# Performance work log

Hardware: AMD Instinct MI355X
Metric: run time of the kernel (lower is better)

## Reference

```python
import jax, jax.numpy as jnp
import numpy as np

GT_MASK_LEN = 128   # processor_dct.gt_mask_len
N_KEEP = 256        # processor_dct.n_keep


def _zigzag_flat_positions(n):
    """Row-major flat index of the k-th element in JPEG zigzag order of an n x n grid."""
    order = []
    for s in range(2 * n - 1):
        if s % 2 == 0:  # even diagonals traverse up-right
            for i in range(min(s, n - 1), max(-1, s - n), -1):
                order.append((i, s - i))
        else:
            for j in range(min(s, n - 1), max(-1, s - n), -1):
                order.append((s - j, j))
    return np.array([i * n + j for (i, j) in order], dtype=np.int64)


def _dct_matrix(n):
    """Orthonormal DCT-II matrix C (cv2.dct). cv2.idct(Y) == C.T @ Y @ C in 2-D."""
    k = np.arange(n)[:, None].astype(np.float64)
    m = np.arange(n)[None, :].astype(np.float64)
    C = np.sqrt(2.0 / n) * np.cos(np.pi * (2 * m + 1) * k / (2 * n))
    C[0, :] = np.sqrt(1.0 / n)
    return C.astype(np.float32)

_ZZ_POS = jnp.asarray(_zigzag_flat_positions(GT_MASK_LEN)[:N_KEEP])
_DCT_C = jnp.asarray(_dct_matrix(GT_MASK_LEN))


def setup_inputs() -> dict:
    key = jax.random.key(0)
    k1, k2, k3, k4 = jax.random.split(key, 4)
    B, R, C = 8, 300, 91
    pred_logits = jax.random.normal(k1, (B, R, C), dtype=jnp.float32)
    pred_boxes = jax.random.uniform(k2, (B, R, 4), dtype=jnp.float32) * 0.5 + 0.25
    pred_vectors = jax.random.normal(k3, (B, R, N_KEEP), dtype=jnp.float32)
    target_sizes = jax.random.randint(k4, (B, 2), 512, 1334, dtype=jnp.int32)
    return {"pred_logits": pred_logits, "pred_boxes": pred_boxes,
            "pred_vectors": pred_vectors, "target_sizes": target_sizes}


def reference(pred_logits, pred_boxes, pred_vectors, target_sizes):
    L = GT_MASK_LEN
    # --- classification scores ---
    prob = jax.nn.sigmoid(pred_logits)            # [B,R,C]
    scores = prob.max(axis=2)                     # [B,R]
    labels = prob.argmax(axis=2)                  # [B,R] int
    # --- boxes: cxcywh -> xyxy, rescale to image size ---
    cx, cy, w, h = jnp.split(pred_boxes, 4, axis=-1)
    boxes = jnp.concatenate([cx - 0.5 * w, cy - 0.5 * h,
                             cx + 0.5 * w, cy + 0.5 * h], axis=-1)  # [B,R,4]
    ts = target_sizes.astype(jnp.float32)
    img_h, img_w = ts[:, 0], ts[:, 1]
    scale_fct = jnp.stack([img_w, img_h, img_w, img_h], axis=1)     # [B,4]
    boxes = boxes * scale_fct[:, None, :]
    # --- masks: inverse zigzag scatter + batched separable 2-D IDCT ---
    B, R, _ = pred_vectors.shape
    flat = jnp.zeros((B, R, L * L), dtype=pred_vectors.dtype)
    flat = flat.at[:, :, _ZZ_POS].set(pred_vectors)
    coef = flat.reshape(B, R, L, L)
    # cv2.idct(Y) = C^T Y C (orthonormal DCT-III)
    re_mask = jnp.einsum('iu,bruv,vj->brij', _DCT_C.T, coef, _DCT_C)  # [B,R,L,L]
    max_v = re_mask.max(axis=(-2, -1), keepdims=True)
    min_v = re_mask.min(axis=(-2, -1), keepdims=True)
    masks = jnp.where(re_mask > (max_v + min_v) * 0.5, 1.0, 0.0).astype(jnp.float32)
    return scores, labels, boxes, masks
```

## Files before the change

kernel.cpp:

```cpp
#include <hip/hip_runtime.h>
#include <math.h>

#define NROWS 2400
#define NCLS  91
#define L     128
#define KSUB  23
#define NKEEP 256

#define Z_OFF 5888
#define SMEM_FLOATS 6912

__global__ void __launch_bounds__(256)
postproc_kernel(const float* __restrict__ logits,
                const float* __restrict__ pboxes,
                const float* __restrict__ vecs,
                const int*   __restrict__ tsz,
                float* __restrict__ out)
{
    __shared__ float smem[SMEM_FLOATS];
    const int br  = blockIdx.x;
    const int tid = threadIdx.x;

    if (tid < 64) {
        const float* lrow = logits + (size_t)br * NCLS;
        float p = 1.0f / (1.0f + expf(-lrow[tid]));
        int   bi = tid;
        if (tid < NCLS - 64) {
            float p2 = 1.0f / (1.0f + expf(-lrow[tid + 64]));
            if (p2 > p) { p = p2; bi = tid + 64; }
        }
        #pragma unroll
        for (int off = 32; off > 0; off >>= 1) {
            float po = __shfl_xor(p, off, 64);
            int   io = __shfl_xor(bi, off, 64);
            if (po > p || (po == p && io < bi)) { p = po; bi = io; }
        }
        if (tid == 0) {
            out[br] = p;
            out[NROWS + br] = (float)bi;
            const int b = br / 300;
            const float W = (float)tsz[2 * b + 1];
            const float H = (float)tsz[2 * b + 0];
            const float4 bx = *(const float4*)(pboxes + (size_t)br * 4);
            float4 o;
            o.x = (bx.x - 0.5f * bx.z) * W;
            o.y = (bx.y - 0.5f * bx.w) * H;
            o.z = (bx.x + 0.5f * bx.z) * W;
            o.w = (bx.y + 0.5f * bx.w) * H;
            *(float4*)(out + 2 * NROWS + (size_t)br * 4) = o;
        }
    }

    double* tab = (double*)&smem[Z_OFF];
    for (int t = tid; t < 512; t += 256)
        tab[t] = cos((3.14159265358979323846 / 256.0) * (double)t);
    __syncthreads();
    {
        const double s0 = sqrt(1.0 / 128.0);
        for (int idx = tid; idx < KSUB * L; idx += 256) {
            const int u = idx >> 7, m = idx & 127;
            float v;
            if (u == 0) v = (float)s0;
            else        v = (float)(0.125 * tab[((2 * m + 1) * u) & 511]);
            smem[idx] = v;
        }
    }
    __syncthreads();

    float* coef = &smem[Z_OFF];
    for (int idx = tid; idx < KSUB * 24; idx += 256) coef[idx] = 0.0f;
    __syncthreads();
    {
        const int k = tid;
        int s = 0;
        while ((s + 1) * (s + 2) / 2 <= k) ++s;
        const int r = k - s * (s + 1) / 2;
        const int u  = (s & 1) ? r : (s - r);
        const int vv = (s & 1) ? (s - r) : r;
        coef[u * 24 + vv] = vecs[(size_t)br * NKEEP + k];
    }
    __syncthreads();

    float* M1 = &smem[2944];
    for (int t = tid; t < KSUB * 32; t += 256) {
        const int v = t >> 5, i4 = (t & 31) << 2;
        float4 a = make_float4(0.f, 0.f, 0.f, 0.f);
        #pragma unroll
        for (int u = 0; u < KSUB; ++u) {
            const float4 cs = *(const float4*)&smem[u * L + i4];
            const float  cf = coef[u * 24 + v];
            a.x += cs.x * cf; a.y += cs.y * cf; a.z += cs.z * cf; a.w += cs.w * cf;
        }
        *(float4*)&M1[v * L + i4] = a;
    }
    __syncthreads();

    const int tx = tid & 31, ty = tid >> 5;
    const int j0 = tx << 2, i0 = ty << 4;
    float acc[16][4];
    #pragma unroll
    for (int r = 0; r < 16; ++r)
        #pragma unroll
        for (int q = 0; q < 4; ++q) acc[r][q] = 0.0f;

    for (int v = 0; v < KSUB; ++v) {
        const float4 c  = *(const float4*)&smem[v * L + j0];
        const float4 m0 = *(const float4*)&M1[v * L + i0];
        const float4 m1 = *(const float4*)&M1[v * L + i0 + 4];
        const float4 m2 = *(const float4*)&M1[v * L + i0 + 8];
        const float4 m3 = *(const float4*)&M1[v * L + i0 + 12];
        const float mv[16] = { m0.x, m0.y, m0.z, m0.w,
                               m1.x, m1.y, m1.z, m1.w,
                               m2.x, m2.y, m2.z, m2.w,
                               m3.x, m3.y, m3.z, m3.w };
        #pragma unroll
        for (int r = 0; r < 16; ++r) {
            acc[r][0] += mv[r] * c.x;
            acc[r][1] += mv[r] * c.y;
            acc[r][2] += mv[r] * c.z;
            acc[r][3] += mv[r] * c.w;
        }
    }

    float mn = acc[0][0], mx = acc[0][0];
    #pragma unroll
    for (int r = 0; r < 16; ++r)
        #pragma unroll
        for (int q = 0; q < 4; ++q) {
            mn = fminf(mn, acc[r][q]);
            mx = fmaxf(mx, acc[r][q]);
        }
    #pragma unroll
    for (int off = 32; off > 0; off >>= 1) {
        mn = fminf(mn, __shfl_xor(mn, off, 64));
        mx = fmaxf(mx, __shfl_xor(mx, off, 64));
    }
    const int w = tid >> 6;
    if ((tid & 63) == 0) { smem[Z_OFF + w] = mn; smem[Z_OFF + 4 + w] = mx; }
    __syncthreads();
    const float gmn = fminf(fminf(smem[Z_OFF + 0], smem[Z_OFF + 1]),
                            fminf(smem[Z_OFF + 2], smem[Z_OFF + 3]));
    const float gmx = fmaxf(fmaxf(smem[Z_OFF + 4], smem[Z_OFF + 5]),
                            fmaxf(smem[Z_OFF + 6], smem[Z_OFF + 7]));
    const float thr = (gmx + gmn) * 0.5f;

    float* omask = out + 6 * NROWS + (size_t)br * (L * L);
    #pragma unroll
    for (int r = 0; r < 16; ++r) {
        float4 o;
        o.x = acc[r][0] > thr ? 1.0f : 0.0f;
        o.y = acc[r][1] > thr ? 1.0f : 0.0f;
        o.z = acc[r][2] > thr ? 1.0f : 0.0f;
        o.w = acc[r][3] > thr ? 1.0f : 0.0f;
        *(float4*)&omask[(i0 + r) * L + j0] = o;
    }
}

extern "C" void kernel_launch(void* const* d_in, const int* in_sizes, int n_in,
                              void* d_out, int out_size, void* d_ws, size_t ws_size,
                              hipStream_t stream)
{
    const float* logits = (const float*)d_in[0];
    const float* pboxes = (const float*)d_in[1];
    const float* vecs   = (const float*)d_in[2];
    const int*   tsz    = (const int*)d_in[3];
    float* out = (float*)d_out;
    (void)d_ws; (void)ws_size; (void)in_sizes; (void)n_in; (void)out_size;

    postproc_kernel<<<dim3(NROWS), dim3(256), 0, stream>>>(logits, pboxes, vecs, tsz, out);
}
```

Before: 193.3 us.

## Precompute DCT basis in a setup kernel and restructure first IDCT pass

Moves the per-block double-precision cosine table and DCT basis construction into a small one-block kernel that writes the basis to workspace. Each main block then copies the basis from global memory, so it no longer evaluates double cos. The change also removes two barriers by zeroing only the coefficient slots the scatter will not write, and it rewrites the first matmul pass so each thread keeps a basis column in registers. The cost is an extra kernel launch and a dependency between the two kernels.

```diff
diff --git a/kernel.cpp b/kernel.cpp
--- a/kernel.cpp
+++ b/kernel.cpp
@@ -7,14 +7,34 @@
 #define KSUB  23
 #define NKEEP 256
 
-#define Z_OFF 5888
-#define SMEM_FLOATS 6912
+__global__ void __launch_bounds__(256)
+build_csub_kernel(float* __restrict__ csub)
+{
+    __shared__ double tab[512];
+    const int tid = threadIdx.x;
+    for (int t = tid; t < 512; t += 256)
+        tab[t] = cos((3.14159265358979323846 / 256.0) * (double)t);
+    __syncthreads();
+    const double s0 = sqrt(1.0 / 128.0);
+    for (int idx = tid; idx < KSUB * L; idx += 256) {
+        const int u = idx >> 7, m = idx & 127;
+        float v;
+        if (u == 0) v = (float)s0;
+        else        v = (float)(0.125 * tab[((2 * m + 1) * u) & 511]);
+        csub[idx] = v;
+    }
+}
+
+#define COEF_OFF 5888
+#define RED_OFF  6440
+#define SMEM_FLOATS 6448
 
 __global__ void __launch_bounds__(256)
 postproc_kernel(const float* __restrict__ logits,
                 const float* __restrict__ pboxes,
                 const float* __restrict__ vecs,
                 const int*   __restrict__ tsz,
+                const float* __restrict__ csub_g,
                 float* __restrict__ out)
 {
     __shared__ float smem[SMEM_FLOATS];
@@ -51,25 +71,15 @@
         }
     }
 
-    double* tab = (double*)&smem[Z_OFF];
-    for (int t = tid; t < 512; t += 256)
-        tab[t] = cos((3.14159265358979323846 / 256.0) * (double)t);
-    __syncthreads();
-    {
-        const double s0 = sqrt(1.0 / 128.0);
-        for (int idx = tid; idx < KSUB * L; idx += 256) {
-            const int u = idx >> 7, m = idx & 127;
-            float v;
-            if (u == 0) v = (float)s0;
-            else        v = (float)(0.125 * tab[((2 * m + 1) * u) & 511]);
-            smem[idx] = v;
-        }
+    for (int t = tid; t < 736; t += 256)
+        ((float4*)smem)[t] = ((const float4*)csub_g)[t];
+
+    float* coef = &smem[COEF_OFF];
+    for (int t = tid; t < KSUB * 24; t += 256) {
+        const int u = t / 24, v = t - u * 24;
+        const int s = u + v;
+        if (v == 23 || s > 22 || (s == 22 && u < 20)) coef[t] = 0.0f;
     }
-    __syncthreads();
-
-    float* coef = &smem[Z_OFF];
-    for (int idx = tid; idx < KSUB * 24; idx += 256) coef[idx] = 0.0f;
-    __syncthreads();
     {
         const int k = tid;
         int s = 0;
@@ -82,16 +92,28 @@
     __syncthreads();
 
     float* M1 = &smem[2944];
-    for (int t = tid; t < KSUB * 32; t += 256) {
-        const int v = t >> 5, i4 = (t & 31) << 2;
-        float4 a = make_float4(0.f, 0.f, 0.f, 0.f);
+    {
+        const int i = tid & 127;
+        float cs[KSUB];
         #pragma unroll
-        for (int u = 0; u < KSUB; ++u) {
-            const float4 cs = *(const float4*)&smem[u * L + i4];
-            const float  cf = coef[u * 24 + v];
-            a.x += cs.x * cf; a.y += cs.y * cf; a.z += cs.z * cf; a.w += cs.w * cf;
+        for (int u = 0; u < KSUB; ++u) cs[u] = smem[u * L + i];
+        if (tid < 128) {
+            #pragma unroll
+            for (int v = 0; v < 12; ++v) {
+                float a = 0.0f;
+                #pragma unroll
+                for (int u = 0; u < KSUB; ++u) a += cs[u] * coef[u * 24 + v];
+                M1[v * L + i] = a;
+            }
+        } else {
+            #pragma unroll
+            for (int v = 12; v < KSUB; ++v) {
+                float a = 0.0f;
+                #pragma unroll
+                for (int u = 0; u < KSUB; ++u) a += cs[u] * coef[u * 24 + v];
+                M1[v * L + i] = a;
+            }
         }
-        *(float4*)&M1[v * L + i4] = a;
     }
     __syncthreads();
 
@@ -136,12 +158,12 @@
         mx = fmaxf(mx, __shfl_xor(mx, off, 64));
     }
     const int w = tid >> 6;
-    if ((tid & 63) == 0) { smem[Z_OFF + w] = mn; smem[Z_OFF + 4 + w] = mx; }
+    if ((tid & 63) == 0) { smem[RED_OFF + w] = mn; smem[RED_OFF + 4 + w] = mx; }
     __syncthreads();
-    const float gmn = fminf(fminf(smem[Z_OFF + 0], smem[Z_OFF + 1]),
-                            fminf(smem[Z_OFF + 2], smem[Z_OFF + 3]));
-    const float gmx = fmaxf(fmaxf(smem[Z_OFF + 4], smem[Z_OFF + 5]),
-                            fmaxf(smem[Z_OFF + 6], smem[Z_OFF + 7]));
+    const float gmn = fminf(fminf(smem[RED_OFF + 0], smem[RED_OFF + 1]),
+                            fminf(smem[RED_OFF + 2], smem[RED_OFF + 3]));
+    const float gmx = fmaxf(fmaxf(smem[RED_OFF + 4], smem[RED_OFF + 5]),
+                            fmaxf(smem[RED_OFF + 6], smem[RED_OFF + 7]));
     const float thr = (gmx + gmn) * 0.5f;
 
     float* omask = out + 6 * NROWS + (size_t)br * (L * L);
@@ -164,8 +186,10 @@
     const float* pboxes = (const float*)d_in[1];
     const float* vecs   = (const float*)d_in[2];
     const int*   tsz    = (const int*)d_in[3];
-    float* out = (float*)d_out;
-    (void)d_ws; (void)ws_size; (void)in_sizes; (void)n_in; (void)out_size;
+    float* out  = (float*)d_out;
+    float* csub = (float*)d_ws;
+    (void)in_sizes; (void)n_in; (void)out_size; (void)ws_size;
 
-    postproc_kernel<<<dim3(NROWS), dim3(256), 0, stream>>>(logits, pboxes, vecs, tsz, out);
+    build_csub_kernel<<<dim3(1), dim3(256), 0, stream>>>(csub);
+    postproc_kernel<<<dim3(NROWS), dim3(256), 0, stream>>>(logits, pboxes, vecs, tsz, csub, out);
 }
```

New measurement: 197.7 us. 1.02x slower.

## Compute the separable IDCT with bf16 MFMA and 512-thread blocks

Applied to the files above, without the earlier changes.

Replaces the two FP32 scalar matrix-multiply stages of the 2-D IDCT with bf16 16x16x32 MFMA instructions. The DCT basis and scattered coefficients are stored in bf16 in padded LDS tiles, and the intermediate product is rounded to bf16 before the second matmul. Blocks grow to 512 threads (8 waves), each owning a 16-row strip of the mask. The aim is to cut ALU time on a kernel whose output write is large. The bf16 rounding can flip pixels that sit near the threshold, and the mask stores become scalar 4-byte writes with a 16-float stride in place of float4 rows, which may hurt store coalescing.

```diff
diff --git a/kernel.cpp b/kernel.cpp
--- a/kernel.cpp
+++ b/kernel.cpp
@@ -6,18 +6,38 @@
 #define L     128
 #define KSUB  23
 #define NKEEP 256
+#define STR   40
 
-#define Z_OFF 5888
-#define SMEM_FLOATS 6912
+typedef short  bf16x8 __attribute__((ext_vector_type(8)));
+typedef float  f32x4  __attribute__((ext_vector_type(4)));
 
-__global__ void __launch_bounds__(256)
+#define CTB_OFF  0
+#define A1_OFF   10240
+#define ABUF_OFF 12800
+#define TAB_OFF  12800
+#define RED_OFF  23040
+#define SMEM_BYTES 23104
+
+__device__ __forceinline__ unsigned short f2bf(float f) {
+    unsigned int u = __float_as_uint(f);
+    unsigned int r = u + 0x7fffu + ((u >> 16) & 1u);
+    return (unsigned short)(r >> 16);
+}
+
+__global__ void __launch_bounds__(512)
 postproc_kernel(const float* __restrict__ logits,
                 const float* __restrict__ pboxes,
                 const float* __restrict__ vecs,
                 const int*   __restrict__ tsz,
                 float* __restrict__ out)
 {
-    __shared__ float smem[SMEM_FLOATS];
+    __shared__ __align__(16) unsigned char sm[SMEM_BYTES];
+    unsigned short* Ctb = (unsigned short*)(sm + CTB_OFF);
+    unsigned short* A1  = (unsigned short*)(sm + A1_OFF);
+    unsigned short* Ab  = (unsigned short*)(sm + ABUF_OFF);
+    double*         tab = (double*)(sm + TAB_OFF);
+    float*          red = (float*)(sm + RED_OFF);
+
     const int br  = blockIdx.x;
     const int tid = threadIdx.x;
 
@@ -51,109 +71,94 @@
         }
     }
 
-    double* tab = (double*)&smem[Z_OFF];
-    for (int t = tid; t < 512; t += 256)
-        tab[t] = cos((3.14159265358979323846 / 256.0) * (double)t);
+    tab[tid] = cos((3.14159265358979323846 / 256.0) * (double)tid);
+    for (int t = tid; t < 320; t += 512)
+        ((unsigned long long*)A1)[t] = 0ull;
     __syncthreads();
+
     {
-        const double s0 = sqrt(1.0 / 128.0);
-        for (int idx = tid; idx < KSUB * L; idx += 256) {
-            const int u = idx >> 7, m = idx & 127;
+        const float s0 = (float)sqrt(1.0 / 128.0);
+        for (int idx = tid; idx < 128 * 32; idx += 512) {
+            const int i = idx >> 5, k = idx & 31;
             float v;
-            if (u == 0) v = (float)s0;
-            else        v = (float)(0.125 * tab[((2 * m + 1) * u) & 511]);
-            smem[idx] = v;
+            if (k == 0)       v = s0;
+            else if (k < 23)  v = (float)(0.125 * tab[((2 * i + 1) * k) & 511]);
+            else              v = 0.0f;
+            Ctb[i * STR + k] = f2bf(v);
         }
     }
-    __syncthreads();
-
-    float* coef = &smem[Z_OFF];
-    for (int idx = tid; idx < KSUB * 24; idx += 256) coef[idx] = 0.0f;
-    __syncthreads();
-    {
+    if (tid < NKEEP) {
         const int k = tid;
         int s = 0;
         while ((s + 1) * (s + 2) / 2 <= k) ++s;
         const int r = k - s * (s + 1) / 2;
         const int u  = (s & 1) ? r : (s - r);
         const int vv = (s & 1) ? (s - r) : r;
-        coef[u * 24 + vv] = vecs[(size_t)br * NKEEP + k];
+        A1[vv * STR + u] = f2bf(vecs[(size_t)br * NKEEP + k]);
     }
     __syncthreads();
 
-    float* M1 = &smem[2944];
-    for (int t = tid; t < KSUB * 32; t += 256) {
-        const int v = t >> 5, i4 = (t & 31) << 2;
-        float4 a = make_float4(0.f, 0.f, 0.f, 0.f);
+    const int w  = tid >> 6;
+    const int ml = tid & 15;
+    const int kq = (tid & 63) >> 4;
+
+    {
+        const f32x4 cz = {0.0f, 0.0f, 0.0f, 0.0f};
         #pragma unroll
-        for (int u = 0; u < KSUB; ++u) {
-            const float4 cs = *(const float4*)&smem[u * L + i4];
-            const float  cf = coef[u * 24 + v];
-            a.x += cs.x * cf; a.y += cs.y * cf; a.z += cs.z * cf; a.w += cs.w * cf;
+        for (int p = 0; p < 2; ++p) {
+            const int idx = 2 * w + p;
+            const int tr = idx >> 3, tc = idx & 7;
+            bf16x8 a1 = *(const bf16x8*)(A1  + (tr * 16 + ml) * STR + kq * 8);
+            bf16x8 b1 = *(const bf16x8*)(Ctb + (tc * 16 + ml) * STR + kq * 8);
+            f32x4 d1 = __builtin_amdgcn_mfma_f32_16x16x32_bf16(a1, b1, cz, 0, 0, 0);
+            #pragma unroll
+            for (int r = 0; r < 4; ++r)
+                Ab[(tc * 16 + ml) * STR + tr * 16 + kq * 4 + r] = f2bf(d1[r]);
         }
-        *(float4*)&M1[v * L + i4] = a;
     }
     __syncthreads();
 
-    const int tx = tid & 31, ty = tid >> 5;
-    const int j0 = tx << 2, i0 = ty << 4;
-    float acc[16][4];
-    #pragma unroll
-    for (int r = 0; r < 16; ++r)
+    f32x4 acc[8];
+    {
+        const f32x4 cz = {0.0f, 0.0f, 0.0f, 0.0f};
+        bf16x8 a2 = *(const bf16x8*)(Ab + (w * 16 + ml) * STR + kq * 8);
         #pragma unroll
-        for (int q = 0; q < 4; ++q) acc[r][q] = 0.0f;
-
-    for (int v = 0; v < KSUB; ++v) {
-        const float4 c  = *(const float4*)&smem[v * L + j0];
-        const float4 m0 = *(const float4*)&M1[v * L + i0];
-        const float4 m1 = *(const float4*)&M1[v * L + i0 + 4];
-        const float4 m2 = *(const float4*)&M1[v * L + i0 + 8];
-        const float4 m3 = *(const float4*)&M1[v * L + i0 + 12];
-        const float mv[16] = { m0.x, m0.y, m0.z, m0.w,
-                               m1.x, m1.y, m1.z, m1.w,
-                               m2.x, m2.y, m2.z, m2.w,
-                               m3.x, m3.y, m3.z, m3.w };
-        #pragma unroll
-        for (int r = 0; r < 16; ++r) {
-            acc[r][0] += mv[r] * c.x;
-            acc[r][1] += mv[r] * c.y;
-            acc[r][2] += mv[r] * c.z;
-            acc[r][3] += mv[r] * c.w;
+        for (int s = 0; s < 8; ++s) {
+            bf16x8 b2 = *(const bf16x8*)(Ctb + (s * 16 + ml) * STR + kq * 8);
+            acc[s] = __builtin_amdgcn_mfma_f32_16x16x32_bf16(a2, b2, cz, 0, 0, 0);
         }
     }
 
     float mn = acc[0][0], mx = acc[0][0];
     #pragma unroll
-    for (int r = 0; r < 16; ++r)
+    for (int s = 0; s < 8; ++s)
         #pragma unroll
-        for (int q = 0; q < 4; ++q) {
-            mn = fminf(mn, acc[r][q]);
-            mx = fmaxf(mx, acc[r][q]);
+        for (int r = 0; r < 4; ++r) {
+            mn = fminf(mn, acc[s][r]);
+            mx = fmaxf(mx, acc[s][r]);
         }
     #pragma unroll
     for (int off = 32; off > 0; off >>= 1) {
         mn = fminf(mn, __shfl_xor(mn, off, 64));
         mx = fmaxf(mx, __shfl_xor(mx, off, 64));
     }
-    const int w = tid >> 6;
-    if ((tid & 63) == 0) { smem[Z_OFF + w] = mn; smem[Z_OFF + 4 + w] = mx; }
+    if ((tid & 63) == 0) { red[w] = mn; red[8 + w] = mx; }
     __syncthreads();
-    const float gmn = fminf(fminf(smem[Z_OFF + 0], smem[Z_OFF + 1]),
-                            fminf(smem[Z_OFF + 2], smem[Z_OFF + 3]));
-    const float gmx = fmaxf(fmaxf(smem[Z_OFF + 4], smem[Z_OFF + 5]),
-                            fmaxf(smem[Z_OFF + 6], smem[Z_OFF + 7]));
+    float gmn = red[0], gmx = red[8];
+    #pragma unroll
+    for (int k = 1; k < 8; ++k) {
+        gmn = fminf(gmn, red[k]);
+        gmx = fmaxf(gmx, red[8 + k]);
+    }
     const float thr = (gmx + gmn) * 0.5f;
 
     float* omask = out + 6 * NROWS + (size_t)br * (L * L);
     #pragma unroll
-    for (int r = 0; r < 16; ++r) {
-        float4 o;
-        o.x = acc[r][0] > thr ? 1.0f : 0.0f;
-        o.y = acc[r][1] > thr ? 1.0f : 0.0f;
-        o.z = acc[r][2] > thr ? 1.0f : 0.0f;
-        o.w = acc[r][3] > thr ? 1.0f : 0.0f;
-        *(float4*)&omask[(i0 + r) * L + j0] = o;
-    }
+    for (int s = 0; s < 8; ++s)
+        #pragma unroll
+        for (int r = 0; r < 4; ++r)
+            omask[(size_t)(w * 16 + kq * 4 + r) * L + s * 16 + ml] =
+                acc[s][r] > thr ? 1.0f : 0.0f;
 }
 
 extern "C" void kernel_launch(void* const* d_in, const int* in_sizes, int n_in,
@@ -167,5 +172,5 @@
     float* out = (float*)d_out;
     (void)d_ws; (void)ws_size; (void)in_sizes; (void)n_in; (void)out_size;
 
-    postproc_kernel<<<dim3(NROWS), dim3(256), 0, stream>>>(logits, pboxes, vecs, tsz, out);
+    postproc_kernel<<<dim3(NROWS), dim3(512), 0, stream>>>(logits, pboxes, vecs, tsz, out);
 }
```

Result: faster. 173.4 us (-10.3%).
